# Performance work log

Measured on AMD Instinct MI355X. Metric: run time of the kernel, lower is better.

## Reference

```python
import jax, jax.numpy as jnp
import numpy as np

M, N, C = 384, 384, 16
DN = ('NCHW', 'OIHW', 'NCHW')

def _rconv(x, w):
    # real-valued 2D cross-correlation, padding=4 (9x9 kernel, SAME)
    return jax.lax.conv_general_dilated(x, w, (1, 1), ((4, 4), (4, 4)), dimension_numbers=DN)

def _cconv(x, w):
    # complex conv2d decomposed into 4 real convs (matches torch complex conv2d)
    xr, xi, wr, wi = x.real, x.imag, w.real, w.imag
    return (_rconv(xr, wr) - _rconv(xi, wi)) + 1j * (_rconv(xr, wi) + _rconv(xi, wr))

def setup_inputs() -> dict:
    key = jax.random.key(0)
    ks = jax.random.split(key, 8)
    shp = (1, M, N, 2 * C)
    kspace = jax.random.normal(ks[0], shp, jnp.float32)
    row_keep = (jax.random.uniform(ks[1], (M,)) < 0.45).astype(jnp.float32)
    kspace = kspace * row_keep[None, :, None, None]
    z = 0.1 * jax.random.normal(ks[2], shp, jnp.float32)
    prev_kspace = 0.1 * jax.random.normal(ks[3], shp, jnp.float32)
    kernel_r = 0.05 * jax.random.normal(ks[4], (1, 81, C, C), jnp.float32)
    kernel_i = 0.05 * jax.random.normal(ks[5], (1, 81, C, C), jnp.float32)
    miu = jnp.array([0.05], jnp.float32)
    spirit_kernels = jnp.zeros((1,), jnp.float32)  # unused by the module's math
    return {"z": z, "kspace": kspace, "kernel_r": kernel_r, "kernel_i": kernel_i,
            "spirit_kernels": spirit_kernels, "prev_kspace": prev_kspace, "miu": miu}

def _forward(z, kspace, kernel_r, kernel_i, prev_kspace, miu):
    divp = kspace.shape[3] // 2
    kk = kspace[0, :, :, :divp] + 1j * kspace[0, :, :, divp:]  # [m,n,C] complex64
    m, n, no_c = kk.shape
    locs = jnp.abs(kk) > 0                                     # sampling mask
    K = (kernel_r[0] + 1j * kernel_i[0]).reshape(9, 9, no_c, no_c)
    # forward SPIRiT weight: Wf[co,ci,p,q] = K[q,p,ci,co]  (torch permute (3,2,1,0))
    Wf = jnp.transpose(K, (3, 2, 1, 0))
    # adjoint weight: conj, spatial flip, swap in/out channels (exact conv_backward_new)
    Wb = jnp.transpose(jnp.conj(jnp.flip(Wf, (2, 3))), (1, 0, 2, 3))

    def G(x, W):  # [m,n,C] -> [m,n,C] via NCHW complex conv
        y = _cconv(jnp.transpose(x, (2, 0, 1))[None], W)
        return jnp.transpose(y[0], (1, 2, 0))

    mask = lambda x: jnp.where(locs, x, 0)  # selection_operator followed by its adjoint

    def ATA(x):  # x: [1,m,n,C]
        x0 = x[0]
        a2 = mask(x0)                # D^T D x
        b1 = G(x0, Wf) - x0          # (G - I) x
        b2 = G(b1, Wb) - b1          # (G - I)^H (G - I) x
        return (a2 + b2)[None]       # rho = 1

    ws = prev_kspace[:, :, :, :divp] + 1j * prev_kspace[:, :, :, divp:]
    zc = z[:, :, :, :divp] + 1j * z[:, :, :, divp:]
    am = jnp.abs(miu[0])
    DTy = mask(kk)[None]             # D^T D y (y = sampled k-space)
    p = DTy + am * zc - ATA(ws) - am * ws
    r = p
    b = ws

    def step(carry, _):
        b, p, r = carry
        q = ATA(p) + am * p
        rr = jnp.sum(r * jnp.conj(r))
        alpha = rr / jnp.sum(q * jnp.conj(p))
        b_n = b + alpha * p
        r_n = r - alpha * q
        p_n = r_n + (jnp.sum(r_n * jnp.conj(r_n)) / rr) * p
        return (b_n, p_n, r_n), None

    (b, _, _), _ = jax.lax.scan(step, (b, p, r), None, length=10)
    return jnp.concatenate([jnp.real(b), jnp.imag(b)], axis=3)

def reference(z, kspace, kernel_r, kernel_i, spirit_kernels, prev_kspace, miu):
    return _forward(z, kspace, kernel_r, kernel_i, prev_kspace, miu)
```

## Files before the change

### kernel.cpp

```cpp
#include <hip/hip_runtime.h>
#include <stdint.h>


#define MM 384
#define NPIX (MM*MM)
#define N2 (16*NPIX)
#define NRED 512
#define NCBLK 768

typedef __attribute__((ext_vector_type(8))) short short8;
typedef __attribute__((ext_vector_type(4))) float f32x4;
typedef unsigned int u32;

__device__ __forceinline__ float2 block_reduce2(float2 v) {
    #pragma unroll
    for (int off = 32; off > 0; off >>= 1) {
        v.x += __shfl_down(v.x, off);
        v.y += __shfl_down(v.y, off);
    }
    __shared__ float2 tmp[8];
    const int wid = threadIdx.x >> 6, lid = threadIdx.x & 63;
    if (lid == 0) tmp[wid] = v;
    __syncthreads();
    if (threadIdx.x == 0) {
        const int nw = blockDim.x >> 6;
        for (int i = 1; i < nw; ++i) { v.x += tmp[i].x; v.y += tmp[i].y; }
    }
    return v;
}

__device__ __forceinline__ u32 bf16rn(float f) {
    const u32 u = __float_as_uint(f);
    return (u + 0x7FFFu + ((u >> 16) & 1u)) >> 16;
}

__global__ void prep_weights(const float* __restrict__ kr, const float* __restrict__ ki,
                             u32* __restrict__ wbuf) {
    const int e = blockIdx.x * 256 + threadIdx.x;
    if (e >= 20736) return;
    const int lane = e & 63;
    int r = e >> 6;
    const int hf = r & 1; r >>= 1;
    const int q = r % 9; r /= 9;
    const int p = r % 9; r /= 9;
    const int dir = r;
    const int co = lane & 15, g = lane >> 4;
    float vv[8];
    #pragma unroll
    for (int t = 0; t < 8; ++t) {
        const int kc = 8 * g + t;
        const int ci = kc & 15;
        const int isI = kc >> 4;
        int sidx;
        if (dir == 0) sidx = (q*9 + p)*256 + ci*16 + co;
        else          sidx = ((8-q)*9 + (8-p))*256 + co*16 + ci;
        const float wr = kr[sidx];
        const float wi = (dir == 0) ? ki[sidx] : -ki[sidx];
        vv[t] = (hf == 0) ? (isI ? -wi : wr) : (isI ? wr : wi);
    }
    u32 pk[4];
    #pragma unroll
    for (int t = 0; t < 4; ++t) pk[t] = bf16rn(vv[2*t]) | (bf16rn(vv[2*t+1]) << 16);
    u32* o = wbuf + (size_t)(dir*162 + (q*9 + p)*2 + hf)*256 + lane*4;
    *(uint4*)o = make_uint4(pk[0], pk[1], pk[2], pk[3]);
}

__global__ void prep_fields(const float* __restrict__ ks, const float* __restrict__ prev,
                            float2* __restrict__ wsf, uint8_t* __restrict__ mask8) {
    const int pix = blockIdx.x * blockDim.x + threadIdx.x;
    if (pix >= NPIX) return;
    #pragma unroll
    for (int c = 0; c < 16; ++c) {
        const float krr = ks[(size_t)pix*32 + c];
        const float kii = ks[(size_t)pix*32 + c + 16];
        mask8[(size_t)c*NPIX + pix] = (krr != 0.f || kii != 0.f) ? 1 : 0;
        wsf[(size_t)c*NPIX + pix] = make_float2(prev[(size_t)pix*32 + c], prev[(size_t)pix*32 + c + 16]);
    }
}

template<int MODE>
__global__ __launch_bounds__(384)
void conv9(const float2* __restrict__ x, const u32* __restrict__ Wd,
           float2* __restrict__ out, float2* __restrict__ out2,
           const float2* __restrict__ aux, const float* __restrict__ ks,
           const float* __restrict__ z, const uint8_t* __restrict__ mask8,
           const float* __restrict__ miu, float2* __restrict__ partials)
{
    __shared__ __align__(16) char Xs[20*24*64];
    const int t = threadIdx.x;
    const int bi = blockIdx.x;
    const int i0 = (bi / 24) * 12;
    const int j0 = (bi % 24) * 16;
    const int w = t >> 6, lane = t & 63;
    const int hf = (w >= 3) ? 1 : 0;
    const int wr = w - 3*hf;
    const int m = lane & 15, g = lane >> 4;

    for (int u = t; u < 20*24; u += 384) {
        const int col = u % 24, row = u / 24;
        const int row_g = i0 - 4 + row, col_g = j0 - 4 + col;
        const bool valid = ((unsigned)row_g < MM) && ((unsigned)col_g < MM);
        const float2* src = x + (size_t)row_g*MM + col_g;
        float2 v[16];
        #pragma unroll
        for (int ci = 0; ci < 16; ++ci)
            v[ci] = valid ? src[(size_t)ci*NPIX] : make_float2(0.f, 0.f);
        u32 c0[4], c1[4], c2[4], c3[4];
        #pragma unroll
        for (int j = 0; j < 4; ++j) {
            c0[j] = bf16rn(v[2*j].x)     | (bf16rn(v[2*j+1].x) << 16);
            c1[j] = bf16rn(v[8+2*j].x)   | (bf16rn(v[9+2*j].x) << 16);
            c2[j] = bf16rn(v[2*j].y)     | (bf16rn(v[2*j+1].y) << 16);
            c3[j] = bf16rn(v[8+2*j].y)   | (bf16rn(v[9+2*j].y) << 16);
        }
        const int k3 = col & 3;
        char* pb = Xs + (size_t)(row*24 + col)*64;
        *(uint4*)(pb + (((0 ^ k3)) << 4)) = make_uint4(c0[0], c0[1], c0[2], c0[3]);
        *(uint4*)(pb + (((1 ^ k3)) << 4)) = make_uint4(c1[0], c1[1], c1[2], c1[3]);
        *(uint4*)(pb + (((2 ^ k3)) << 4)) = make_uint4(c2[0], c2[1], c2[2], c2[3]);
        *(uint4*)(pb + (((3 ^ k3)) << 4)) = make_uint4(c3[0], c3[1], c3[2], c3[3]);
    }
    __syncthreads();

    f32x4 acc[4];
    #pragma unroll
    for (int a = 0; a < 4; ++a) acc[a] = (f32x4){0.f, 0.f, 0.f, 0.f};

    const char* wl = (const char*)Wd + (lane << 4) + (hf << 10);
    short8 WA, WB, WC;

    #define LW(WS, ADDR) do { WS = *(const short8*)(ADDR); } while (0)

    #define MFQ(Xa, Xb, Xc, Xd, WS) do { \
        acc[0] = __builtin_amdgcn_mfma_f32_16x16x32_bf16(WS, Xa, acc[0], 0, 0, 0); \
        acc[1] = __builtin_amdgcn_mfma_f32_16x16x32_bf16(WS, Xb, acc[1], 0, 0, 0); \
        acc[2] = __builtin_amdgcn_mfma_f32_16x16x32_bf16(WS, Xc, acc[2], 0, 0, 0); \
        acc[3] = __builtin_amdgcn_mfma_f32_16x16x32_bf16(WS, Xd, acc[3], 0, 0, 0); } while (0)

    LW(WA, wl);
    LW(WB, wl + 2048);
    LW(WC, wl + 4096);

    #pragma unroll 1
    for (int qq = 0; qq < 9; ++qq) {
        const char* wq = wl + (size_t)qq * 18432;
        const int colq = m + qq;
        const char* xb = Xs + (size_t)((4*wr)*24 + colq)*64 + ((g ^ (colq & 3)) << 4);
        short8 X0 = *(const short8*)(xb);
        short8 X1 = *(const short8*)(xb + 1536);
        short8 X2 = *(const short8*)(xb + 2*1536);
        short8 X3 = *(const short8*)(xb + 3*1536);
        short8 X4;
        X4 = *(const short8*)(xb + 4*1536);  MFQ(X0, X1, X2, X3, WA); LW(WA, wq + 3*2048);
        X0 = *(const short8*)(xb + 5*1536);  MFQ(X1, X2, X3, X4, WB); LW(WB, wq + 4*2048);
        X1 = *(const short8*)(xb + 6*1536);  MFQ(X2, X3, X4, X0, WC); LW(WC, wq + 5*2048);
        X2 = *(const short8*)(xb + 7*1536);  MFQ(X3, X4, X0, X1, WA); LW(WA, wq + 6*2048);
        X3 = *(const short8*)(xb + 8*1536);  MFQ(X4, X0, X1, X2, WB); LW(WB, wq + 7*2048);
        X4 = *(const short8*)(xb + 9*1536);  MFQ(X0, X1, X2, X3, WC); LW(WC, wq + 8*2048);
        X0 = *(const short8*)(xb + 10*1536); MFQ(X1, X2, X3, X4, WA); LW(WA, wq + 9*2048);
        X1 = *(const short8*)(xb + 11*1536); MFQ(X2, X3, X4, X0, WB); LW(WB, wq + 10*2048);
                                             MFQ(X3, X4, X0, X1, WC); LW(WC, wq + 11*2048);
    }
    #undef LW
    #undef MFQ

    const float am = (MODE >= 1) ? fabsf(miu[0]) : 0.f;
    float2 part = make_float2(0.f, 0.f);
    const float* xf  = (const float*)x;
    const float* axf = (const float*)aux;
    float* of  = (float*)out;
    float* o2f = (float*)out2;
    #pragma unroll
    for (int r = 0; r < 4; ++r) {
        const int rowo = i0 + 4*wr + r;
        const int colo = j0 + m;
        const int pix = rowo*MM + colo;
        #pragma unroll
        for (int j = 0; j < 4; ++j) {
            const int co = g*4 + j;
            const size_t idx = (size_t)co*NPIX + pix;
            const float v = acc[r][j];
            if (MODE == 0) {
                of[2*idx + hf] = v - xf[2*idx + hf];
            } else if (MODE == 1) {
                const float tc = xf[2*idx + hf];
                const float2 pc = aux[idx];
                const float pc_c = hf ? pc.y : pc.x;
                const float mv = mask8[idx] ? 1.f : 0.f;
                const float qc = v - tc + (mv + am)*pc_c;
                of[2*idx + hf] = qc;
                part.x += qc * pc_c;
                part.y += hf ? qc * pc.x : -qc * pc.y;
            } else {
                const float tc = xf[2*idx + hf];
                const float wc = axf[2*idx + hf];
                const float mv = mask8[idx] ? 1.f : 0.f;
                const float kc = ks[(size_t)pix*32 + co + 16*hf];
                const float zc = z[(size_t)pix*32 + co + 16*hf];
                const float pc = mv*kc + am*zc - (v - tc) - (mv + am)*wc;
                of[2*idx + hf]  = pc;
                o2f[2*idx + hf] = pc;
                part.x += pc * pc;
            }
        }
    }
    if (MODE >= 1) {
        __syncthreads();
        part = block_reduce2(part);
        if (t == 0) partials[bi] = part;
    }
}

__global__ void finalize_rr(const float2* __restrict__ partials, float* __restrict__ scal, int n) {
    float2 s = make_float2(0.f, 0.f);
    for (int i = threadIdx.x; i < n; i += blockDim.x) { s.x += partials[i].x; s.y += partials[i].y; }
    s = block_reduce2(s);
    if (threadIdx.x == 0) scal[0] = s.x;
}

__global__ void finalize_alpha(const float2* __restrict__ partials, float* __restrict__ scal, int n) {
    float2 s = make_float2(0.f, 0.f);
    for (int i = threadIdx.x; i < n; i += blockDim.x) { s.x += partials[i].x; s.y += partials[i].y; }
    s = block_reduce2(s);
    if (threadIdx.x == 0) {
        const float rr = scal[0];
        const float d = s.x*s.x + s.y*s.y;
        scal[1] =  rr * s.x / d;
        scal[2] = -rr * s.y / d;
    }
}

__global__ void update_r(float2* __restrict__ r, const float2* __restrict__ q,
                         const float* __restrict__ scal, float2* __restrict__ partials) {
    const float ar = scal[1], ai = scal[2];
    float2 s = make_float2(0.f, 0.f);
    for (int e = blockIdx.x*256 + threadIdx.x; e < N2; e += NRED*256) {
        const float2 qv = q[e];
        float2 rv = r[e];
        rv.x -= ar*qv.x - ai*qv.y;
        rv.y -= ar*qv.y + ai*qv.x;
        r[e] = rv;
        s.x += rv.x*rv.x + rv.y*rv.y;
    }
    s = block_reduce2(s);
    if (threadIdx.x == 0) partials[blockIdx.x] = s;
}

__global__ void finalize_beta(const float2* __restrict__ partials, float* __restrict__ scal) {
    float2 v = partials[threadIdx.x];
    v = block_reduce2(v);
    if (threadIdx.x == 0) {
        const float rn = v.x;
        scal[3] = rn / scal[0];
        scal[0] = rn;
    }
}

__global__ void update_pb(float2* __restrict__ p, const float2* __restrict__ r,
                          float2* __restrict__ b, const float* __restrict__ scal) {
    const float ar = scal[1], ai = scal[2], beta = scal[3];
    const int e = blockIdx.x*256 + threadIdx.x;
    if (e < N2) {
        const float2 pv = p[e], rv = r[e];
        float2 bv = b[e];
        bv.x += ar*pv.x - ai*pv.y;
        bv.y += ar*pv.y + ai*pv.x;
        b[e] = bv;
        p[e] = make_float2(rv.x + beta*pv.x, rv.y + beta*pv.y);
    }
}

__global__ void pack_out(const float2* __restrict__ b, float* __restrict__ out) {
    const int e = blockIdx.x*256 + threadIdx.x;
    if (e >= 32*NPIX) return;
    const int pix = e >> 5;
    const int cc  = e & 31;
    const float2 v = b[(size_t)(cc & 15)*NPIX + pix];
    out[e] = (cc < 16) ? v.x : v.y;
}

extern "C" void kernel_launch(void* const* d_in, const int* in_sizes, int n_in,
                              void* d_out, int out_size, void* d_ws, size_t ws_size,
                              hipStream_t stream) {
    const float* z    = (const float*)d_in[0];
    const float* ks   = (const float*)d_in[1];
    const float* kr   = (const float*)d_in[2];
    const float* ki   = (const float*)d_in[3];
    const float* prev = (const float*)d_in[5];
    const float* miu  = (const float*)d_in[6];
    float* out = (float*)d_out;

    char* w = (char*)d_ws;
    const size_t FB = (size_t)N2 * sizeof(float2);
    float2* wsf = (float2*)w; w += FB;
    float2* pf  = (float2*)w; w += FB;
    float2* rf  = (float2*)w; w += FB;
    float2* qf  = (float2*)w; w += FB;
    float2* tf  = (float2*)w; w += FB;
    u32* wbuf   = (u32*)w;   w += (size_t)2*162*256*sizeof(u32);
    uint8_t* mask8 = (uint8_t*)w; w += (size_t)N2;
    w = (char*)(((uintptr_t)w + 255) & ~(uintptr_t)255);
    float2* partials = (float2*)w; w += (size_t)NCBLK * sizeof(float2);
    float*  scal     = (float*)w;

    const u32* wbF = wbuf;
    const u32* wbB = wbuf + (size_t)162*256;

    prep_weights<<<81, 256, 0, stream>>>(kr, ki, wbuf);
    prep_fields<<<576, 256, 0, stream>>>(ks, prev, wsf, mask8);

    conv9<0><<<NCBLK, 384, 0, stream>>>(wsf, wbF, tf, nullptr, nullptr, nullptr, nullptr, nullptr, nullptr, nullptr);
    conv9<2><<<NCBLK, 384, 0, stream>>>(tf, wbB, pf, rf, wsf, ks, z, mask8, miu, partials);
    finalize_rr<<<1, 256, 0, stream>>>(partials, scal, NCBLK);

    for (int it = 0; it < 10; ++it) {
        conv9<0><<<NCBLK, 384, 0, stream>>>(pf, wbF, tf, nullptr, nullptr, nullptr, nullptr, nullptr, nullptr, nullptr);
        conv9<1><<<NCBLK, 384, 0, stream>>>(tf, wbB, qf, nullptr, pf, nullptr, nullptr, mask8, miu, partials);
        finalize_alpha<<<1, 256, 0, stream>>>(partials, scal, NCBLK);
        update_r<<<NRED, 256, 0, stream>>>(rf, qf, scal, partials);
        finalize_beta<<<1, NRED, 0, stream>>>(partials, scal);
        update_pb<<<9216, 256, 0, stream>>>(pf, rf, wsf, scal);
    }

    pack_out<<<18432, 256, 0, stream>>>(wsf, out);
}
```

Baseline: 1.143 ms.

## Register-cache conv weights, prefetch next column inputs, swizzle blocks, trim last CG update

The 9x9 conv inner loop now keeps all nine weight fragments and six input fragments in registers. Each qq column's loads are issued while the previous column's MFMAs run, and the next column's first input rows are prefetched, which should hide LDS and global load latency. Block indices are remapped across groups of eight, likely to spread tiles across XCDs or caches, and launch bounds now request 5 waves per SIMD. On the last CG iteration the r/beta/p updates are skipped and only b is updated, which drops work whose result is never read. The extra live registers may hurt occupancy or cause spills.

```diff
diff --git a/kernel.cpp b/kernel.cpp
--- a/kernel.cpp
+++ b/kernel.cpp
@@ -79,7 +79,7 @@
 }
 
 template<int MODE>
-__global__ __launch_bounds__(384)
+__global__ __launch_bounds__(384, 5)
 void conv9(const float2* __restrict__ x, const u32* __restrict__ Wd,
            float2* __restrict__ out, float2* __restrict__ out2,
            const float2* __restrict__ aux, const float* __restrict__ ks,
@@ -88,7 +88,8 @@
 {
     __shared__ __align__(16) char Xs[20*24*64];
     const int t = threadIdx.x;
-    const int bi = blockIdx.x;
+    const int bi0 = blockIdx.x;
+    const int bi = (bi0 & 7) * 96 + (bi0 >> 3);
     const int i0 = (bi / 24) * 12;
     const int j0 = (bi % 24) * 16;
     const int w = t >> 6, lane = t & 63;
@@ -127,39 +128,48 @@
     for (int a = 0; a < 4; ++a) acc[a] = (f32x4){0.f, 0.f, 0.f, 0.f};
 
     const char* wl = (const char*)Wd + (lane << 4) + (hf << 10);
-    short8 WA, WB, WC;
+    short8 W0, W1, W2, W3, W4, W5, W6, W7, W8;
+    short8 X0, X1, X2, X3, X4, X5;
 
     #define LW(WS, ADDR) do { WS = *(const short8*)(ADDR); } while (0)
-
     #define MFQ(Xa, Xb, Xc, Xd, WS) do { \
         acc[0] = __builtin_amdgcn_mfma_f32_16x16x32_bf16(WS, Xa, acc[0], 0, 0, 0); \
         acc[1] = __builtin_amdgcn_mfma_f32_16x16x32_bf16(WS, Xb, acc[1], 0, 0, 0); \
         acc[2] = __builtin_amdgcn_mfma_f32_16x16x32_bf16(WS, Xc, acc[2], 0, 0, 0); \
         acc[3] = __builtin_amdgcn_mfma_f32_16x16x32_bf16(WS, Xd, acc[3], 0, 0, 0); } while (0)
 
-    LW(WA, wl);
-    LW(WB, wl + 2048);
-    LW(WC, wl + 4096);
+    LW(W0, wl);            LW(W1, wl + 2048);   LW(W2, wl + 4096);
+    LW(W3, wl + 6144);     LW(W4, wl + 8192);   LW(W5, wl + 10240);
+    LW(W6, wl + 12288);    LW(W7, wl + 14336);  LW(W8, wl + 16384);
+    {
+        const char* xb0 = Xs + (size_t)((4*wr)*24 + m)*64 + ((g ^ (m & 3)) << 4);
+        X0 = *(const short8*)(xb0);
+        X1 = *(const short8*)(xb0 + 1536);
+        X2 = *(const short8*)(xb0 + 2*1536);
+        X3 = *(const short8*)(xb0 + 3*1536);
+        X4 = *(const short8*)(xb0 + 4*1536);
+    }
 
     #pragma unroll 1
     for (int qq = 0; qq < 9; ++qq) {
-        const char* wq = wl + (size_t)qq * 18432;
+        const char* wq = wl + (size_t)qq * 18432 + 18432;
         const int colq = m + qq;
-        const char* xb = Xs + (size_t)((4*wr)*24 + colq)*64 + ((g ^ (colq & 3)) << 4);
-        short8 X0 = *(const short8*)(xb);
-        short8 X1 = *(const short8*)(xb + 1536);
-        short8 X2 = *(const short8*)(xb + 2*1536);
-        short8 X3 = *(const short8*)(xb + 3*1536);
-        short8 X4;
-        X4 = *(const short8*)(xb + 4*1536);  MFQ(X0, X1, X2, X3, WA); LW(WA, wq + 3*2048);
-        X0 = *(const short8*)(xb + 5*1536);  MFQ(X1, X2, X3, X4, WB); LW(WB, wq + 4*2048);
-        X1 = *(const short8*)(xb + 6*1536);  MFQ(X2, X3, X4, X0, WC); LW(WC, wq + 5*2048);
-        X2 = *(const short8*)(xb + 7*1536);  MFQ(X3, X4, X0, X1, WA); LW(WA, wq + 6*2048);
-        X3 = *(const short8*)(xb + 8*1536);  MFQ(X4, X0, X1, X2, WB); LW(WB, wq + 7*2048);
-        X4 = *(const short8*)(xb + 9*1536);  MFQ(X0, X1, X2, X3, WC); LW(WC, wq + 8*2048);
-        X0 = *(const short8*)(xb + 10*1536); MFQ(X1, X2, X3, X4, WA); LW(WA, wq + 9*2048);
-        X1 = *(const short8*)(xb + 11*1536); MFQ(X2, X3, X4, X0, WB); LW(WB, wq + 10*2048);
-                                             MFQ(X3, X4, X0, X1, WC); LW(WC, wq + 11*2048);
+        const char* xb  = Xs + (size_t)((4*wr)*24 + colq)*64 + ((g ^ (colq & 3)) << 4);
+        const int colq1 = colq + 1;
+        const char* xbn = Xs + (size_t)((4*wr)*24 + colq1)*64 + ((g ^ (colq1 & 3)) << 4);
+
+        MFQ(X0, X1, X2, X3, W0); LW(W0, wq);           X5 = *(const short8*)(xb + 5*1536);
+        MFQ(X1, X2, X3, X4, W1); LW(W1, wq + 2048);    X0 = *(const short8*)(xb + 6*1536);
+        MFQ(X2, X3, X4, X5, W2); LW(W2, wq + 4096);    X1 = *(const short8*)(xb + 7*1536);
+        MFQ(X3, X4, X5, X0, W3); LW(W3, wq + 6144);    X2 = *(const short8*)(xb + 8*1536);
+        MFQ(X4, X5, X0, X1, W4); LW(W4, wq + 8192);    X3 = *(const short8*)(xb + 9*1536);
+        MFQ(X5, X0, X1, X2, W5); LW(W5, wq + 10240);   X4 = *(const short8*)(xb + 10*1536);
+        MFQ(X0, X1, X2, X3, W6); LW(W6, wq + 12288);   X5 = *(const short8*)(xb + 11*1536);
+        MFQ(X1, X2, X3, X4, W7); LW(W7, wq + 14336);   X0 = *(const short8*)(xbn);
+        MFQ(X2, X3, X4, X5, W8); LW(W8, wq + 16384);   X1 = *(const short8*)(xbn + 1536);
+        X2 = *(const short8*)(xbn + 2*1536);
+        X3 = *(const short8*)(xbn + 3*1536);
+        X4 = *(const short8*)(xbn + 4*1536);
     }
     #undef LW
     #undef MFQ
@@ -270,6 +280,19 @@
     }
 }
 
+__global__ void update_bfinal(float2* __restrict__ b, const float2* __restrict__ p,
+                              const float* __restrict__ scal) {
+    const float ar = scal[1], ai = scal[2];
+    const int e = blockIdx.x*256 + threadIdx.x;
+    if (e < N2) {
+        const float2 pv = p[e];
+        float2 bv = b[e];
+        bv.x += ar*pv.x - ai*pv.y;
+        bv.y += ar*pv.y + ai*pv.x;
+        b[e] = bv;
+    }
+}
+
 __global__ void pack_out(const float2* __restrict__ b, float* __restrict__ out) {
     const int e = blockIdx.x*256 + threadIdx.x;
     if (e >= 32*NPIX) return;
@@ -317,9 +340,13 @@
         conv9<0><<<NCBLK, 384, 0, stream>>>(pf, wbF, tf, nullptr, nullptr, nullptr, nullptr, nullptr, nullptr, nullptr);
         conv9<1><<<NCBLK, 384, 0, stream>>>(tf, wbB, qf, nullptr, pf, nullptr, nullptr, mask8, miu, partials);
         finalize_alpha<<<1, 256, 0, stream>>>(partials, scal, NCBLK);
-        update_r<<<NRED, 256, 0, stream>>>(rf, qf, scal, partials);
-        finalize_beta<<<1, NRED, 0, stream>>>(partials, scal);
-        update_pb<<<9216, 256, 0, stream>>>(pf, rf, wsf, scal);
+        if (it < 9) {
+            update_r<<<NRED, 256, 0, stream>>>(rf, qf, scal, partials);
+            finalize_beta<<<1, NRED, 0, stream>>>(partials, scal);
+            update_pb<<<9216, 256, 0, stream>>>(pf, rf, wsf, scal);
+        } else {
+            update_bfinal<<<9216, 256, 0, stream>>>(wsf, pf, scal);
+        }
     }
 
     pack_out<<<18432, 256, 0, stream>>>(wsf, out);
```

New measurement: 1.023 ms. 10.5% less time.
